# Optimization experiments

Hardware: AMD Instinct MI355X
Metric: run time of the kernel (lower is better)

The kernel has to match this reference:

```python
import jax, jax.numpy as jnp
import numpy as np

C_IN = 12      # total channels (rgb-noised + hidden)
C_NOISE = 3    # noise-prediction channels
HID = 128      # rule-MLP hidden size
PERC = 48      # perception channels (depthwise, 48/12 = 4 filters per channel)
TDIM = 256     # sinusoidal time-embedding dim


def setup_inputs() -> dict:
    key = jax.random.key(0)
    ks = jax.random.split(key, 12)
    B, H, W = 16, 256, 256
    x = jax.random.normal(ks[0], (B, C_NOISE, H, W), jnp.float32)
    hidden_channels = jax.random.normal(ks[1], (B, C_IN - C_NOISE, H, W), jnp.float32)
    t = jax.random.randint(ks[2], (B,), 0, 1000)
    # depthwise 3x3 perceive conv: torch weight shape [out=48, in/groups=1, 3, 3]
    w_perceive = jax.random.normal(ks[3], (PERC, 1, 3, 3), jnp.float32) * 0.1
    b_perceive = jax.random.normal(ks[4], (PERC,), jnp.float32) * 0.01
    # 1x1 convs of the rule network, stored as [out, in]
    w1 = jax.random.normal(ks[5], (HID, PERC), jnp.float32) * 0.1
    b1 = jax.random.normal(ks[6], (HID,), jnp.float32) * 0.01
    w2 = jax.random.normal(ks[7], (HID, HID), jnp.float32) * 0.05
    b2 = jax.random.normal(ks[8], (HID,), jnp.float32) * 0.01
    # conv3 is zero-initialized in the original; random here for test coverage
    w3 = jax.random.normal(ks[9], (C_IN, HID), jnp.float32) * 0.05
    # time embedding Linear(256 -> c_noise)
    w_time = jax.random.normal(ks[10], (C_NOISE, TDIM), jnp.float32) * 0.1
    b_time = jax.random.normal(ks[11], (C_NOISE,), jnp.float32) * 0.01
    return dict(x=x, hidden_channels=hidden_channels, t=t,
                w_perceive=w_perceive, b_perceive=b_perceive,
                w1=w1, b1=b1, w2=w2, b2=b2, w3=w3,
                w_time=w_time, b_time=b_time)


def _pos_encoding(t, channels):
    # t: [B] int -> [B, channels] sinusoidal embedding (torch repeat-then-scale layout)
    inv_freq = 1.0 / (10000.0 ** (jnp.arange(0, channels, 2, dtype=jnp.float32) / channels))
    ang = t.astype(jnp.float32)[:, None] * inv_freq  # [B, channels//2]
    return jnp.concatenate([jnp.sin(ang), jnp.cos(ang)], axis=-1)


def reference(x, hidden_channels, t, w_perceive, b_perceive, w1, b1, w2, b2, w3, w_time, b_time):
    # concat noised channels with hidden state channels -> [B, 12, H, W]
    xf = jnp.concatenate([x, hidden_channels], axis=1)
    # depthwise 3x3 conv, 'same' padding, groups = C_IN
    perc = jax.lax.conv_general_dilated(
        xf, w_perceive, window_strides=(1, 1), padding='SAME',
        feature_group_count=C_IN,
        dimension_numbers=('NCHW', 'OIHW', 'NCHW')) + b_perceive[None, :, None, None]
    # rule network: three 1x1 convs (pointwise MLP) with ReLUs
    h = jax.nn.relu(jnp.einsum('bchw,oc->bohw', perc, w1) + b1[None, :, None, None])
    h = jax.nn.relu(jnp.einsum('bchw,oc->bohw', h, w2) + b2[None, :, None, None])
    out = jnp.einsum('bchw,oc->bohw', h, w3)  # no bias
    # time embedding: sinusoidal -> SiLU -> Linear -> broadcast over H, W
    pe = _pos_encoding(t, TDIM)                       # [B, 256]
    emb = jax.nn.silu(pe) @ w_time.T + b_time         # [B, 3]
    noise_prediction = out[:, :C_NOISE] + emb[:, :, None, None]
    hidden_out = out[:, C_NOISE:]
    return (hidden_out, noise_prediction)
```

## Files before the change

kernel.cpp:

```cpp
#include <hip/hip_runtime.h>


#define ACT_S 136
#define PERC_S 72
#define NOISE_BASE 9437184

#define WSF_OFF 13312
#define WSF_BP 0
#define WSF_B1 48
#define WSF_B2 176
#define WSF_WP 304
#define WSF_EMB 736

typedef short bf16x8 __attribute__((ext_vector_type(8)));
typedef short short4v __attribute__((ext_vector_type(4)));
typedef float f32x4 __attribute__((ext_vector_type(4)));

__device__ __forceinline__ short f2bf(float f) {
    union { float f; unsigned u; } cv; cv.f = f;
    unsigned r = cv.u + 0x7FFFu + ((cv.u >> 16) & 1u);
    return (short)(r >> 16);
}

__global__ void prep_emb_kernel(const float* __restrict__ wpg, const float* __restrict__ bpg,
                                const float* __restrict__ w1g, const float* __restrict__ b1g,
                                const float* __restrict__ w2g, const float* __restrict__ b2g,
                                const float* __restrict__ w3g,
                                const int* __restrict__ t,
                                const float* __restrict__ wt, const float* __restrict__ bt,
                                short* __restrict__ wsb, float* __restrict__ wsf)
{
    if (blockIdx.x < 107) {
        int i = blockIdx.x * 256 + threadIdx.x;
        if (i < 8192) {
            int o = i >> 6, c = i & 63;
            wsb[i] = (c < 48) ? f2bf(w1g[o * 48 + c]) : (short)0;
        } else if (i < 24576) {
            wsb[i] = f2bf(w2g[i - 8192]);
        } else if (i < 26624) {
            int k = i - 24576;
            wsb[i] = (k < 1536) ? f2bf(w3g[k]) : (short)0;
        } else if (i < 26672) {
            wsf[WSF_BP + (i - 26624)] = bpg[i - 26624];
        } else if (i < 26800) {
            wsf[WSF_B1 + (i - 26672)] = b1g[i - 26672];
        } else if (i < 26928) {
            wsf[WSF_B2 + (i - 26800)] = b2g[i - 26800];
        } else if (i < 27360) {
            wsf[WSF_WP + (i - 26928)] = wpg[i - 26928];
        }
        return;
    }
    int b = blockIdx.x - 107;
    int lane = threadIdx.x;
    if (lane >= 64) return;
    float tv = (float)t[b];
    float s0 = 0.f, s1 = 0.f, s2 = 0.f;
    const float LOG1E4 = 9.210340371976184f;
    #pragma unroll
    for (int ii = 0; ii < 2; ++ii) {
        int i = lane + ii * 64;
        float invf = __expf(-LOG1E4 * (float)i * (1.0f / 128.0f));
        float ang = tv * invf;
        float sn = sinf(ang), cs = cosf(ang);
        float ss = sn / (1.0f + __expf(-sn));
        float sc = cs / (1.0f + __expf(-cs));
        s0 += ss * wt[0 * 256 + i] + sc * wt[0 * 256 + i + 128];
        s1 += ss * wt[1 * 256 + i] + sc * wt[1 * 256 + i + 128];
        s2 += ss * wt[2 * 256 + i] + sc * wt[2 * 256 + i + 128];
    }
    #pragma unroll
    for (int off = 32; off; off >>= 1) {
        s0 += __shfl_down(s0, off);
        s1 += __shfl_down(s1, off);
        s2 += __shfl_down(s2, off);
    }
    if (lane == 0) {
        wsf[WSF_EMB + b * 3 + 0] = s0 + bt[0];
        wsf[WSF_EMB + b * 3 + 1] = s1 + bt[1];
        wsf[WSF_EMB + b * 3 + 2] = s2 + bt[2];
    }
}

__global__ __launch_bounds__(256, 3) void canet_main(
    const float* __restrict__ xg,
    const float* __restrict__ hg,
    const short* __restrict__ wsb,
    const float* __restrict__ wsf,
    float* __restrict__ outg)
{
    __shared__ __align__(16) short percS[64 * PERC_S];
    __shared__ __align__(16) short h1S[64 * ACT_S];
    __shared__ __align__(16) short h2S[64 * ACT_S];
    __shared__ float wp_s[48 * 9];
    __shared__ float bp_s[48];

    const int tid = threadIdx.x;
    const int b = blockIdx.x >> 8;
    const int y = blockIdx.x & 255;

    for (int i = tid; i < 432; i += 256) wp_s[i] = wsf[WSF_WP + i];
    if (tid < 48) bp_s[tid] = wsf[WSF_BP + tid];

    const int wv = tid >> 6;
    const int lane = tid & 63;
    const int m = lane & 15;
    const int q = lane >> 4;

    bf16x8 w1f[2][2], w2f[2][4], w3f[4];
    #pragma unroll
    for (int j = 0; j < 2; ++j) {
        int n = wv * 32 + j * 16 + m;
        #pragma unroll
        for (int ks = 0; ks < 2; ++ks)
            w1f[j][ks] = *(const bf16x8*)(wsb + n * 64 + ks * 32 + q * 8);
        #pragma unroll
        for (int ks = 0; ks < 4; ++ks)
            w2f[j][ks] = *(const bf16x8*)(wsb + 8192 + n * 128 + ks * 32 + q * 8);
    }
    #pragma unroll
    for (int ks = 0; ks < 4; ++ks)
        w3f[ks] = *(const bf16x8*)(wsb + 24576 + m * 128 + ks * 32 + q * 8);

    const float b1v0 = wsf[WSF_B1 + wv * 32 + m];
    const float b1v1 = wsf[WSF_B1 + wv * 32 + 16 + m];
    const float b2v0 = wsf[WSF_B2 + wv * 32 + m];
    const float b2v1 = wsf[WSF_B2 + wv * 32 + 16 + m];
    const float embv = (m < 3) ? wsf[WSF_EMB + b * 3 + m] : 0.0f;

    __syncthreads();

    for (int it = 0; it < 4; ++it) {
        const int x0 = it * 64;

        {
            const int px = x0 + wv * 16 + m;
            short* prow = percS + (wv * 16 + m) * PERC_S;
            #pragma unroll
            for (int i3 = 0; i3 < 3; ++i3) {
                int ic = 3 * q + i3;
                const float* src = (ic < 3)
                    ? (xg + (((size_t)b * 3 + ic) << 16))
                    : (hg + (((size_t)b * 9 + (ic - 3)) << 16));
                float tap[9];
                #pragma unroll
                for (int ky = 0; ky < 3; ++ky) {
                    int yy = y + ky - 1;
                    bool yok = (yy >= 0) && (yy < 256);
                    #pragma unroll
                    for (int kx = 0; kx < 3; ++kx) {
                        int xx = px + kx - 1;
                        bool ok = yok && (xx >= 0) && (xx < 256);
                        tap[ky * 3 + kx] = ok ? src[yy * 256 + xx] : 0.0f;
                    }
                }
                short4v pk;
                #pragma unroll
                for (int r = 0; r < 4; ++r) {
                    int oc = ic * 4 + r;
                    float a = bp_s[oc];
                    const float* wp = &wp_s[oc * 9];
                    #pragma unroll
                    for (int k9 = 0; k9 < 9; ++k9) a += tap[k9] * wp[k9];
                    pk[r] = f2bf(a);
                }
                *(short4v*)(prow + 12 * q + 4 * i3) = pk;
            }
            *(short4v*)(prow + 48 + 4 * q) = short4v{0, 0, 0, 0};
        }
        __syncthreads();

        #pragma unroll
        for (int mb = 0; mb < 4; ++mb) {
            f32x4 a0 = {b1v0, b1v0, b1v0, b1v0};
            f32x4 a1 = {b1v1, b1v1, b1v1, b1v1};
            #pragma unroll
            for (int ks = 0; ks < 2; ++ks) {
                bf16x8 a = *(const bf16x8*)(percS + (mb * 16 + m) * PERC_S + ks * 32 + q * 8);
                a0 = __builtin_amdgcn_mfma_f32_16x16x32_bf16(a, w1f[0][ks], a0, 0, 0, 0);
                a1 = __builtin_amdgcn_mfma_f32_16x16x32_bf16(a, w1f[1][ks], a1, 0, 0, 0);
            }
            #pragma unroll
            for (int r = 0; r < 4; ++r) {
                int row = mb * 16 + q * 4 + r;
                h1S[row * ACT_S + wv * 32 + m]      = f2bf(fmaxf(a0[r], 0.0f));
                h1S[row * ACT_S + wv * 32 + 16 + m] = f2bf(fmaxf(a1[r], 0.0f));
            }
        }
        __syncthreads();

        #pragma unroll
        for (int mb = 0; mb < 4; ++mb) {
            f32x4 a0 = {b2v0, b2v0, b2v0, b2v0};
            f32x4 a1 = {b2v1, b2v1, b2v1, b2v1};
            #pragma unroll
            for (int ks = 0; ks < 4; ++ks) {
                bf16x8 a = *(const bf16x8*)(h1S + (mb * 16 + m) * ACT_S + ks * 32 + q * 8);
                a0 = __builtin_amdgcn_mfma_f32_16x16x32_bf16(a, w2f[0][ks], a0, 0, 0, 0);
                a1 = __builtin_amdgcn_mfma_f32_16x16x32_bf16(a, w2f[1][ks], a1, 0, 0, 0);
            }
            #pragma unroll
            for (int r = 0; r < 4; ++r) {
                int row = mb * 16 + q * 4 + r;
                h2S[row * ACT_S + wv * 32 + m]      = f2bf(fmaxf(a0[r], 0.0f));
                h2S[row * ACT_S + wv * 32 + 16 + m] = f2bf(fmaxf(a1[r], 0.0f));
            }
        }
        __syncthreads();

        {
            f32x4 acc = {0.f, 0.f, 0.f, 0.f};
            #pragma unroll
            for (int ks = 0; ks < 4; ++ks) {
                bf16x8 a = *(const bf16x8*)(h2S + (wv * 16 + m) * ACT_S + ks * 32 + q * 8);
                acc = __builtin_amdgcn_mfma_f32_16x16x32_bf16(a, w3f[ks], acc, 0, 0, 0);
            }
            if (m < 12) {
                #pragma unroll
                for (int r = 0; r < 4; ++r) {
                    int xx = x0 + wv * 16 + q * 4 + r;
                    float v = acc[r];
                    size_t idx;
                    if (m < 3) {
                        v += embv;
                        idx = (size_t)NOISE_BASE + (((size_t)b * 3 + m) << 16) + (size_t)y * 256 + xx;
                    } else {
                        idx = (((size_t)b * 9 + (m - 3)) << 16) + (size_t)y * 256 + xx;
                    }
                    outg[idx] = v;
                }
            }
        }
    }
}

extern "C" void kernel_launch(void* const* d_in, const int* in_sizes, int n_in,
                              void* d_out, int out_size, void* d_ws, size_t ws_size,
                              hipStream_t stream) {
    const float* xg  = (const float*)d_in[0];
    const float* hg  = (const float*)d_in[1];
    const int*   tg  = (const int*)  d_in[2];
    const float* wpg = (const float*)d_in[3];
    const float* bpg = (const float*)d_in[4];
    const float* w1g = (const float*)d_in[5];
    const float* b1g = (const float*)d_in[6];
    const float* w2g = (const float*)d_in[7];
    const float* b2g = (const float*)d_in[8];
    const float* w3g = (const float*)d_in[9];
    const float* wtg = (const float*)d_in[10];
    const float* btg = (const float*)d_in[11];
    float* outg = (float*)d_out;
    short* wsb  = (short*)d_ws;
    float* wsf  = (float*)d_ws + WSF_OFF;

    prep_emb_kernel<<<123, 256, 0, stream>>>(wpg, bpg, w1g, b1g, w2g, b2g, w3g,
                                             tg, wtg, btg, wsb, wsf);
    canet_main<<<4096, 256, 0, stream>>>(xg, hg, wsb, wsf, outg);
}
```

Measured before the change: 229.7 us.

## Transpose MLP MFMAs for packed bf16 stores and vectorize conv taps and output

Swaps the MFMA operand order in the two hidden layers so each lane holds four consecutive channels of one pixel. Those can be packed into bf16 pairs with a perm instruction and written as 8-byte LDS stores instead of scalar short stores. The depthwise conv gets branch-light interior tap loads with clamped indices and padded 12-wide weight rows read as float4. The final output is written as one float4 store per lane. The new bf16 packing rounds half-up instead of round-to-nearest-even, which slightly changes numerics.

Result: no change. 226.8 us (-1.3%).

```diff
diff --git a/kernel.cpp b/kernel.cpp
--- a/kernel.cpp
+++ b/kernel.cpp
@@ -13,13 +13,16 @@
 #define WSF_EMB 736
 
 typedef short bf16x8 __attribute__((ext_vector_type(8)));
-typedef short short4v __attribute__((ext_vector_type(4)));
 typedef float f32x4 __attribute__((ext_vector_type(4)));
 
 __device__ __forceinline__ short f2bf(float f) {
     union { float f; unsigned u; } cv; cv.f = f;
     unsigned r = cv.u + 0x7FFFu + ((cv.u >> 16) & 1u);
     return (short)(r >> 16);
+}
+__device__ __forceinline__ unsigned pk2bf(float f0, float f1) {
+    union { float f; unsigned u; } a, b; a.f = f0; b.f = f1;
+    return __builtin_amdgcn_perm(b.u + 0x8000u, a.u + 0x8000u, 0x07060302u);
 }
 
 __global__ void prep_emb_kernel(const float* __restrict__ wpg, const float* __restrict__ bpg,
@@ -92,14 +95,17 @@
     __shared__ __align__(16) short percS[64 * PERC_S];
     __shared__ __align__(16) short h1S[64 * ACT_S];
     __shared__ __align__(16) short h2S[64 * ACT_S];
-    __shared__ float wp_s[48 * 9];
+    __shared__ __align__(16) float wp_s[48 * 12];
     __shared__ float bp_s[48];
 
     const int tid = threadIdx.x;
     const int b = blockIdx.x >> 8;
     const int y = blockIdx.x & 255;
 
-    for (int i = tid; i < 432; i += 256) wp_s[i] = wsf[WSF_WP + i];
+    for (int i = tid; i < 576; i += 256) {
+        int oc = i / 12, k = i % 12;
+        wp_s[i] = (k < 9) ? wsf[WSF_WP + oc * 9 + k] : 0.0f;
+    }
     if (tid < 48) bp_s[tid] = wsf[WSF_BP + tid];
 
     const int wv = tid >> 6;
@@ -122,89 +128,118 @@
     for (int ks = 0; ks < 4; ++ks)
         w3f[ks] = *(const bf16x8*)(wsb + 24576 + m * 128 + ks * 32 + q * 8);
 
-    const float b1v0 = wsf[WSF_B1 + wv * 32 + m];
-    const float b1v1 = wsf[WSF_B1 + wv * 32 + 16 + m];
-    const float b2v0 = wsf[WSF_B2 + wv * 32 + m];
-    const float b2v1 = wsf[WSF_B2 + wv * 32 + 16 + m];
+    f32x4 b1v[2], b2v[2];
+    #pragma unroll
+    for (int j = 0; j < 2; ++j) {
+        b1v[j] = *(const f32x4*)(wsf + WSF_B1 + wv * 32 + j * 16 + q * 4);
+        b2v[j] = *(const f32x4*)(wsf + WSF_B2 + wv * 32 + j * 16 + q * 4);
+    }
     const float embv = (m < 3) ? wsf[WSF_EMB + b * 3 + m] : 0.0f;
+
+    const float* src3[3];
+    #pragma unroll
+    for (int i3 = 0; i3 < 3; ++i3) {
+        int ic = 3 * q + i3;
+        src3[i3] = (ic < 3) ? (xg + (((size_t)b * 3 + ic) << 16))
+                            : (hg + (((size_t)b * 9 + (ic - 3)) << 16));
+    }
 
     __syncthreads();
 
     for (int it = 0; it < 4; ++it) {
         const int x0 = it * 64;
+        const int px = x0 + wv * 16 + m;
 
         {
-            const int px = x0 + wv * 16 + m;
+            const int xm1 = px - (px > 0);
+            const int xp1 = px + (px < 255);
+            const bool okl = (px > 0), okr = (px < 255);
             short* prow = percS + (wv * 16 + m) * PERC_S;
+            const bool interior = (y >= 1) && (y <= 254);
             #pragma unroll
             for (int i3 = 0; i3 < 3; ++i3) {
-                int ic = 3 * q + i3;
-                const float* src = (ic < 3)
-                    ? (xg + (((size_t)b * 3 + ic) << 16))
-                    : (hg + (((size_t)b * 9 + (ic - 3)) << 16));
+                const float* s = src3[i3];
                 float tap[9];
-                #pragma unroll
-                for (int ky = 0; ky < 3; ++ky) {
-                    int yy = y + ky - 1;
-                    bool yok = (yy >= 0) && (yy < 256);
+                if (interior) {
                     #pragma unroll
-                    for (int kx = 0; kx < 3; ++kx) {
-                        int xx = px + kx - 1;
-                        bool ok = yok && (xx >= 0) && (xx < 256);
-                        tap[ky * 3 + kx] = ok ? src[yy * 256 + xx] : 0.0f;
+                    for (int ky = 0; ky < 3; ++ky) {
+                        const float* rp = s + (y + ky - 1) * 256;
+                        float c0 = rp[xm1], c1 = rp[px], c2 = rp[xp1];
+                        tap[ky * 3 + 0] = okl ? c0 : 0.0f;
+                        tap[ky * 3 + 1] = c1;
+                        tap[ky * 3 + 2] = okr ? c2 : 0.0f;
+                    }
+                } else {
+                    #pragma unroll
+                    for (int ky = 0; ky < 3; ++ky) {
+                        int yy = y + ky - 1;
+                        bool yok = (yy >= 0) && (yy < 256);
+                        const float* rp = s + (yok ? yy : y) * 256;
+                        float c0 = rp[xm1], c1 = rp[px], c2 = rp[xp1];
+                        tap[ky * 3 + 0] = (yok && okl) ? c0 : 0.0f;
+                        tap[ky * 3 + 1] = yok ? c1 : 0.0f;
+                        tap[ky * 3 + 2] = (yok && okr) ? c2 : 0.0f;
                     }
                 }
-                short4v pk;
+                float v[4];
                 #pragma unroll
                 for (int r = 0; r < 4; ++r) {
-                    int oc = ic * 4 + r;
+                    int oc = 12 * q + 4 * i3 + r;
+                    const float* wrow = &wp_s[oc * 12];
+                    f32x4 w0 = *(const f32x4*)wrow;
+                    f32x4 w1_ = *(const f32x4*)(wrow + 4);
                     float a = bp_s[oc];
-                    const float* wp = &wp_s[oc * 9];
-                    #pragma unroll
-                    for (int k9 = 0; k9 < 9; ++k9) a += tap[k9] * wp[k9];
-                    pk[r] = f2bf(a);
+                    a += w0[0] * tap[0] + w0[1] * tap[1] + w0[2] * tap[2] + w0[3] * tap[3];
+                    a += w1_[0] * tap[4] + w1_[1] * tap[5] + w1_[2] * tap[6] + w1_[3] * tap[7];
+                    a += wrow[8] * tap[8];
+                    v[r] = a;
                 }
-                *(short4v*)(prow + 12 * q + 4 * i3) = pk;
-            }
-            *(short4v*)(prow + 48 + 4 * q) = short4v{0, 0, 0, 0};
+                uint2 pk;
+                pk.x = pk2bf(v[0], v[1]);
+                pk.y = pk2bf(v[2], v[3]);
+                *(uint2*)(prow + 12 * q + 4 * i3) = pk;
+            }
+            *(uint2*)(prow + 48 + 4 * q) = uint2{0u, 0u};
         }
         __syncthreads();
 
         #pragma unroll
-        for (int mb = 0; mb < 4; ++mb) {
-            f32x4 a0 = {b1v0, b1v0, b1v0, b1v0};
-            f32x4 a1 = {b1v1, b1v1, b1v1, b1v1};
+        for (int nt = 0; nt < 4; ++nt) {
+            f32x4 c0 = b1v[0], c1 = b1v[1];
             #pragma unroll
             for (int ks = 0; ks < 2; ++ks) {
-                bf16x8 a = *(const bf16x8*)(percS + (mb * 16 + m) * PERC_S + ks * 32 + q * 8);
-                a0 = __builtin_amdgcn_mfma_f32_16x16x32_bf16(a, w1f[0][ks], a0, 0, 0, 0);
-                a1 = __builtin_amdgcn_mfma_f32_16x16x32_bf16(a, w1f[1][ks], a1, 0, 0, 0);
-            }
-            #pragma unroll
-            for (int r = 0; r < 4; ++r) {
-                int row = mb * 16 + q * 4 + r;
-                h1S[row * ACT_S + wv * 32 + m]      = f2bf(fmaxf(a0[r], 0.0f));
-                h1S[row * ACT_S + wv * 32 + 16 + m] = f2bf(fmaxf(a1[r], 0.0f));
-            }
+                bf16x8 p = *(const bf16x8*)(percS + (nt * 16 + m) * PERC_S + ks * 32 + q * 8);
+                c0 = __builtin_amdgcn_mfma_f32_16x16x32_bf16(w1f[0][ks], p, c0, 0, 0, 0);
+                c1 = __builtin_amdgcn_mfma_f32_16x16x32_bf16(w1f[1][ks], p, c1, 0, 0, 0);
+            }
+            short* drow = h1S + (nt * 16 + m) * ACT_S + wv * 32 + q * 4;
+            uint2 pk;
+            pk.x = pk2bf(fmaxf(c0[0], 0.f), fmaxf(c0[1], 0.f));
+            pk.y = pk2bf(fmaxf(c0[2], 0.f), fmaxf(c0[3], 0.f));
+            *(uint2*)drow = pk;
+            pk.x = pk2bf(fmaxf(c1[0], 0.f), fmaxf(c1[1], 0.f));
+            pk.y = pk2bf(fmaxf(c1[2], 0.f), fmaxf(c1[3], 0.f));
+            *(uint2*)(drow + 16) = pk;
         }
         __syncthreads();
 
         #pragma unroll
-        for (int mb = 0; mb < 4; ++mb) {
-            f32x4 a0 = {b2v0, b2v0, b2v0, b2v0};
-            f32x4 a1 = {b2v1, b2v1, b2v1, b2v1};
+        for (int nt = 0; nt < 4; ++nt) {
+            f32x4 c0 = b2v[0], c1 = b2v[1];
             #pragma unroll
             for (int ks = 0; ks < 4; ++ks) {
-                bf16x8 a = *(const bf16x8*)(h1S + (mb * 16 + m) * ACT_S + ks * 32 + q * 8);
-                a0 = __builtin_amdgcn_mfma_f32_16x16x32_bf16(a, w2f[0][ks], a0, 0, 0, 0);
-                a1 = __builtin_amdgcn_mfma_f32_16x16x32_bf16(a, w2f[1][ks], a1, 0, 0, 0);
-            }
-            #pragma unroll
-            for (int r = 0; r < 4; ++r) {
-                int row = mb * 16 + q * 4 + r;
-                h2S[row * ACT_S + wv * 32 + m]      = f2bf(fmaxf(a0[r], 0.0f));
-                h2S[row * ACT_S + wv * 32 + 16 + m] = f2bf(fmaxf(a1[r], 0.0f));
-            }
+                bf16x8 a = *(const bf16x8*)(h1S + (nt * 16 + m) * ACT_S + ks * 32 + q * 8);
+                c0 = __builtin_amdgcn_mfma_f32_16x16x32_bf16(w2f[0][ks], a, c0, 0, 0, 0);
+                c1 = __builtin_amdgcn_mfma_f32_16x16x32_bf16(w2f[1][ks], a, c1, 0, 0, 0);
+            }
+            short* drow = h2S + (nt * 16 + m) * ACT_S + wv * 32 + q * 4;
+            uint2 pk;
+            pk.x = pk2bf(fmaxf(c0[0], 0.f), fmaxf(c0[1], 0.f));
+            pk.y = pk2bf(fmaxf(c0[2], 0.f), fmaxf(c0[3], 0.f));
+            *(uint2*)drow = pk;
+            pk.x = pk2bf(fmaxf(c1[0], 0.f), fmaxf(c1[1], 0.f));
+            pk.y = pk2bf(fmaxf(c1[2], 0.f), fmaxf(c1[3], 0.f));
+            *(uint2*)(drow + 16) = pk;
         }
         __syncthreads();
 
@@ -216,19 +251,15 @@
                 acc = __builtin_amdgcn_mfma_f32_16x16x32_bf16(a, w3f[ks], acc, 0, 0, 0);
             }
             if (m < 12) {
-                #pragma unroll
-                for (int r = 0; r < 4; ++r) {
-                    int xx = x0 + wv * 16 + q * 4 + r;
-                    float v = acc[r];
-                    size_t idx;
-                    if (m < 3) {
-                        v += embv;
-                        idx = (size_t)NOISE_BASE + (((size_t)b * 3 + m) << 16) + (size_t)y * 256 + xx;
-                    } else {
-                        idx = (((size_t)b * 9 + (m - 3)) << 16) + (size_t)y * 256 + xx;
-                    }
-                    outg[idx] = v;
+                int xx0 = x0 + wv * 16 + q * 4;
+                size_t idx;
+                if (m < 3) {
+                    idx = (size_t)NOISE_BASE + (((size_t)b * 3 + m) << 16) + (size_t)y * 256 + xx0;
+                } else {
+                    idx = (((size_t)b * 9 + (m - 3)) << 16) + (size_t)y * 256 + xx0;
                 }
+                f32x4 vst = {acc[0] + embv, acc[1] + embv, acc[2] + embv, acc[3] + embv};
+                *(f32x4*)(outg + idx) = vst;
             }
         }
     }
```
